# Optimization experiments

Hardware: AMD Instinct MI355X
Metric: run time of the kernel (lower is better)

## Reference

```python
import jax, jax.numpy as jnp
import numpy as np

NUM_BINS = 36
EPS = 1e-12
BASE_DROP, MIN_DROP, MAX_DROP = 0.3, 0.1, 0.6
SENSITIVITY, NORMAL_APE = 4.0, 0.78


def _hann(n):
    # torch.hann_window default (periodic=True): 0.5*(1 - cos(2*pi*k/N))
    return 0.5 - 0.5 * jnp.cos(2.0 * jnp.pi * jnp.arange(n, dtype=jnp.float32) / n)


def compute_ape(images):
    B, C, H, W = images.shape
    mean = jnp.array([0.485, 0.456, 0.406], dtype=images.dtype).reshape(1, 3, 1, 1)
    std = jnp.array([0.229, 0.224, 0.225], dtype=images.dtype).reshape(1, 3, 1, 1)
    wts = jnp.array([0.2989, 0.587, 0.114], dtype=images.dtype).reshape(1, 3, 1, 1)
    gray = ((images * std + mean) * wts).sum(axis=1)  # (B,H,W)
    gray = gray - gray.mean(axis=(1, 2), keepdims=True)
    gray = gray * (_hann(H)[:, None] * _hann(W)[None, :])
    P = jnp.abs(jnp.fft.fft2(gray)) ** 2
    P = jnp.fft.fftshift(P, axes=(1, 2))
    cy, cx = (H - 1) / 2.0, (W - 1) / 2.0
    yy = jnp.arange(H, dtype=jnp.float32)[:, None] - cy
    xx = jnp.arange(W, dtype=jnp.float32)[None, :] - cx
    r = jnp.sqrt(xx ** 2 + yy ** 2)
    theta = (jnp.arctan2(yy, xx) + 2 * jnp.pi) % (2 * jnp.pi)
    r_max = r.max()
    radial_mask = (r >= 0.05 * r_max) & (r <= 0.95 * r_max)
    bin_width = 2 * jnp.pi / NUM_BINS
    idx = jnp.clip((theta / bin_width).astype(jnp.int32), 0, NUM_BINS - 1)  # (H,W)
    # batched masked angular histogram: one segment_sum over B*NUM_BINS segments
    Pm = (P * radial_mask).reshape(B, -1)
    seg = (idx.reshape(-1)[None, :] + NUM_BINS * jnp.arange(B)[:, None]).reshape(-1)
    energy = jax.ops.segment_sum(Pm.reshape(-1), seg, num_segments=B * NUM_BINS)
    energy = energy.reshape(B, NUM_BINS)
    total = energy.sum(axis=1, keepdims=True)
    p = energy / (total + EPS)
    H_theta = -(p * jnp.log(p + EPS)).sum(axis=1)
    ape = jnp.clip(H_theta / np.log(NUM_BINS), 0.0, 1.0)
    return jnp.where(total[:, 0] <= EPS, 0.0, ape)


def ape_to_dropout_prob(ape):
    adj = jnp.tanh((NORMAL_APE - ape) * SENSITIVITY)
    drop = jnp.where(adj >= 0,
                     BASE_DROP + adj * (MAX_DROP - BASE_DROP),
                     BASE_DROP + adj * (BASE_DROP - MIN_DROP))
    return jnp.clip(drop, MIN_DROP, MAX_DROP)


def adaptive_dropout(x, probs, key):
    # per-sample dropout: mask ~ Bernoulli(1-p), scale by 1/(1-p+1e-8)
    p = probs[:, None, None]
    keep = jax.random.bernoulli(key, 1.0 - p, x.shape).astype(x.dtype)
    out = x * keep / (1.0 - p + 1e-8)
    return jnp.where(p > 0, out, x)


def setup_inputs() -> dict:
    key = jax.random.key(0)
    k1, k2, k3, k4 = jax.random.split(key, 4)
    B, N, D, Hf = 64, 256, 768, 768
    images = jax.random.uniform(k1, (B, 3, 448, 448), dtype=jnp.float32)
    x = jax.random.normal(k2, (B, N, D), dtype=jnp.float32)
    w1 = jax.random.normal(k3, (Hf, D), dtype=jnp.float32) * (1.0 / np.sqrt(D))
    w2 = jax.random.normal(k4, (D, Hf), dtype=jnp.float32) * (1.0 / np.sqrt(Hf))
    return {"images": images, "x": x, "w1": w1, "w2": w2}


def reference(images, x, w1, w2):
    ape = compute_ape(images)
    probs = jax.lax.stop_gradient(ape_to_dropout_prob(ape))  # torch casts to python float -> detached
    k0, k1, k2 = jax.random.split(jax.random.key(1), 3)
    h = adaptive_dropout(x, probs, k0)            # input dropout
    h = jnp.einsum('bnd,hd->bnh', h, w1)          # fc1 (bias=False)
    h = jax.nn.gelu(h, approximate=False)         # nn.GELU (exact erf)
    h = adaptive_dropout(h, probs, k1)
    y = jnp.einsum('bnh,dh->bnd', h, w2)          # fc2 (bias=False)
    y = adaptive_dropout(y, probs, k2)
    return y
```

## Files before the change

### kernel.cpp

```cpp
#include <hip/hip_runtime.h>
#include <stdint.h>
#include <math.h>

typedef __attribute__((ext_vector_type(8))) short short8;
typedef __attribute__((ext_vector_type(4))) float floatx4;

#define IMGN 448
#define HW   200704
#define NBATCH 64
#define NBINS 36

#define MFMA(a, b, c) __builtin_amdgcn_mfma_f32_16x16x32_bf16((a), (b), (c), 0, 0, 0)

#define WAITBAR8() asm volatile("s_waitcnt vmcnt(8)\ns_barrier" ::: "memory")
#define WAITBAR6() asm volatile("s_waitcnt vmcnt(6)\ns_barrier" ::: "memory")
#define WAITBAR0() asm volatile("s_waitcnt vmcnt(0)\ns_barrier" ::: "memory")
#define ENDBAR()   asm volatile("s_waitcnt lgkmcnt(0)\ns_barrier" ::: "memory")

#define WS_WIN   0u
#define WS_BINS  4096u
#define WS_TS    24576u
#define WS_BIDX  32768u
#define WS_TW    1048576u
#define TWSZ     401408u
#define WS_W     4194304u
#define WSZ      1179648u
#define WS_REG1  16777216u
#define GSZ      25690112u
#define CBSZ     13762560u
#define XSZ      25165824u
#define WS_REG2  75497472u

__host__ __device__ __forceinline__ uint32_t rotl32(uint32_t v, int r) {
  return (v << r) | (v >> (32 - r));
}
__host__ __device__ __forceinline__ void tf2x32(uint32_t k0, uint32_t k1,
                                                uint32_t x0, uint32_t x1,
                                                uint32_t &o0, uint32_t &o1) {
  uint32_t k2 = k0 ^ k1 ^ 0x1BD11BDAu;
  uint32_t v0 = x0 + k0, v1 = x1 + k1;
#define TFR(r) { v0 += v1; v1 = rotl32(v1, r); v1 ^= v0; }
  TFR(13) TFR(15) TFR(26) TFR(6)   v0 += k1; v1 += k2 + 1u;
  TFR(17) TFR(29) TFR(16) TFR(24)  v0 += k2; v1 += k0 + 2u;
  TFR(13) TFR(15) TFR(26) TFR(6)   v0 += k0; v1 += k1 + 3u;
  TFR(17) TFR(29) TFR(16) TFR(24)  v0 += k1; v1 += k2 + 4u;
  TFR(13) TFR(15) TFR(26) TFR(6)   v0 += k2; v1 += k0 + 5u;
#undef TFR
  o0 = v0; o1 = v1;
}
__device__ __forceinline__ float tf_uniform(uint32_t k0, uint32_t k1, uint32_t idx) {
  uint32_t a, b;
  tf2x32(k0, k1, 0u, idx, a, b);
  uint32_t bits = a ^ b;
  return __uint_as_float((bits >> 9) | 0x3F800000u) - 1.0f;
}

__device__ __forceinline__ unsigned short bf16rne(float v) {
  unsigned u = __float_as_uint(v);
  return (unsigned short)((u + 0x7fffu + ((u >> 16) & 1u)) >> 16);
}
__device__ __forceinline__ void split2(float v, unsigned short &h, unsigned short &l) {
  h = bf16rne(v);
  float fh = __uint_as_float(((unsigned)h) << 16);
  l = bf16rne(v - fh);
}

__device__ __forceinline__ float fast_erf(float x) {
  float ax = fabsf(x);
  float t = 1.0f / (1.0f + 0.3275911f * ax);
  float p = t * (0.254829592f + t * (-0.284496736f + t * (1.421413741f +
            t * (-1.453152027f + t * 1.061405429f))));
  float y = 1.0f - p * __expf(-ax * ax);
  return __uint_as_float((__float_as_uint(y) & 0x7fffffffu) |
                         (__float_as_uint(x) & 0x80000000u));
}

__device__ __forceinline__ void gload16(const void *g, void *l) {
  __builtin_amdgcn_global_load_lds(
      (const __attribute__((address_space(1))) unsigned int *)g,
      (__attribute__((address_space(3))) unsigned int *)l, 16, 0, 0);
}

__global__ __launch_bounds__(256) void k_prep(float *__restrict__ win,
                                              double *__restrict__ bins,
                                              uint8_t *__restrict__ bidx) {
  int t = blockIdx.x * 256 + threadIdx.x;
  int a = t / IMGN, b = t % IMGN;
  double yy = (double)((a + 224) % IMGN) - 223.5;
  double xx = (double)((b + 224) % IMGN) - 223.5;
  double r2 = xx * xx + yy * yy;
  uint8_t idx = 255;
  if (r2 >= 249.76125 && r2 <= 90163.81125) {
    double th = atan2(yy, xx);
    if (th < 0.0) th += 6.283185307179586476925286766559;
    int i = (int)(th / 0.17453292519943295769236907684886);
    if (i > 35) i = 35;
    if (i < 0) i = 0;
    idx = (uint8_t)i;
  }
  bidx[t] = idx;
  if (t < IMGN) {
    double ang = 6.283185307179586476925286766559 * (double)t / 448.0;
    win[t] = (float)(0.5 - 0.5 * cos(ang));
  }
  if (t < NBATCH * NBINS) bins[t] = 0.0;
}

__global__ __launch_bounds__(256) void k_tw(short8 *__restrict__ tch, short8 *__restrict__ tcl,
                                            short8 *__restrict__ tsh, short8 *__restrict__ tsl) {
  int wid = blockIdx.x * 256 + threadIdx.x;
  int lane = wid & 63;
  int tmp = wid >> 6;
  int kb = tmp % 14, mb = tmp / 14;
  int m = mb * 16 + (lane & 15);
  int k0 = kb * 32 + (lane >> 4) * 8;
  short8 ch, cl, sh, sl;
#pragma unroll
  for (int e = 0; e < 8; ++e) {
    int mm = (m * (k0 + e)) % IMGN;
    double ang = -6.283185307179586476925286766559 * (double)mm / 448.0;
    float c = (float)cos(ang), s = (float)sin(ang);
    unsigned short h, l;
    split2(c, h, l); ch[e] = (short)h; cl[e] = (short)l;
    split2(s, h, l); sh[e] = (short)h; sl[e] = (short)l;
  }
  tch[wid] = ch; tcl[wid] = cl; tsh[wid] = sh; tsl[wid] = sl;
}

__global__ __launch_bounds__(256) void k_wconv(const float *__restrict__ w1, const float *__restrict__ w2,
                                               short8 *__restrict__ w1h, short8 *__restrict__ w1l,
                                               short8 *__restrict__ w2h, short8 *__restrict__ w2l) {
  int wid = blockIdx.x * 256 + threadIdx.x;
  const float *src = blockIdx.y ? w2 : w1;
  short8 *dh = blockIdx.y ? w2h : w1h;
  short8 *dl = blockIdx.y ? w2l : w1l;
  int lane = wid & 63;
  int tmp = wid >> 6;
  int kb = tmp % 24, nb = tmp / 24;
  int n = nb * 16 + (lane & 15);
  int k0 = kb * 32 + (lane >> 4) * 8;
  const float *p = src + (size_t)n * 768 + k0;
  short8 vh, vl;
#pragma unroll
  for (int e = 0; e < 8; ++e) {
    unsigned short h, l;
    split2(p[e], h, l);
    vh[e] = (short)h; vl[e] = (short)l;
  }
  dh[wid] = vh; dl[wid] = vl;
}

__global__ __launch_bounds__(256) void k_gprep(const float *__restrict__ img, const float *__restrict__ win,
                                               short8 *__restrict__ gh, short8 *__restrict__ gl) {
  int wid = blockIdx.x * 256 + threadIdx.x;
  int lane = wid & 63;
  int tmp = wid >> 6;
  int kb = tmp % 14, nb = tmp / 14;
  int n = nb * 16 + (lane & 15);
  int b = n / 448, y = n % 448;
  int x0 = kb * 32 + (lane >> 4) * 8;
  const float *p = img + (size_t)b * 3 * HW + y * IMGN + x0;
  float wy = win[y];
  short8 vh, vl;
#pragma unroll
  for (int e = 0; e < 8; ++e) {
    float r = p[e], g = p[HW + e], bl = p[2 * HW + e];
    float t0 = (r * 0.229f + 0.485f) * 0.2989f;
    float t1 = (g * 0.224f + 0.456f) * 0.587f;
    float t2 = (bl * 0.225f + 0.406f) * 0.114f;
    float v = ((t0 + t1) + t2) * wy * win[x0 + e];
    unsigned short h, l;
    split2(v, h, l);
    vh[e] = (short)h; vl[e] = (short)l;
  }
  gh[wid] = vh; gl[wid] = vl;
}

__global__ __launch_bounds__(256) void k_rows(const short8 *__restrict__ tch, const short8 *__restrict__ tcl,
                                              const short8 *__restrict__ tsh, const short8 *__restrict__ tsl,
                                              const short8 *__restrict__ gh, const short8 *__restrict__ gl,
                                              short8 *__restrict__ crh, short8 *__restrict__ crl,
                                              short8 *__restrict__ cih, short8 *__restrict__ cil) {
  __shared__ short8 S[512];
  int orig = blockIdx.x;
  int swz = (orig & 7) * 224 + (orig >> 3);
  int mtg = swz & 3, ntg = swz >> 2;
  int tid = threadIdx.x;
  int lane = tid & 63, w = tid >> 6;
  int g = lane >> 4, c = lane & 15;
  int mt = mtg * 4 + w;
  floatx4 s_c[4] = {}, s_s[4] = {};
  for (int kb = 0; kb < 14; ++kb) {
#pragma unroll
    for (int i = 0; i < 2; ++i) {
      int ch = w * 2 + i;
      const short8 *m0 = (ch >> 2) ? gl : gh;
      int row = ntg * 4 + (ch & 3);
      gload16(m0 + ((size_t)row * 14 + kb) * 64 + lane, (char *)S + ch * 1024);
    }
    int ao = (mt * 14 + kb) * 64 + lane;
    short8 ach = tch[ao], acl = tcl[ao], ash = tsh[ao], asl = tsl[ao];
    __syncthreads();
#pragma unroll
    for (int nt = 0; nt < 4; ++nt) {
      short8 bh = S[nt * 64 + lane];
      short8 bl = S[(4 + nt) * 64 + lane];
      s_c[nt] = MFMA(ach, bh, s_c[nt]);
      s_c[nt] = MFMA(ach, bl, s_c[nt]);
      s_c[nt] = MFMA(acl, bh, s_c[nt]);
      s_s[nt] = MFMA(ash, bh, s_s[nt]);
      s_s[nt] = MFMA(ash, bl, s_s[nt]);
      s_s[nt] = MFMA(asl, bh, s_s[nt]);
    }
    __syncthreads();
  }
#pragma unroll
  for (int nt = 0; nt < 4; ++nt) {
    int nrow = (ntg * 4 + nt) * 16 + c;
    int b = nrow / 448, y = nrow % 448;
    int kb2 = y >> 5;
    int lofs = 16 * ((y & 31) >> 3);
    int e2 = y & 7;
#pragma unroll
    for (int r = 0; r < 4; ++r) {
      int v = mt * 16 + 4 * g + r;
      if (v < 240) {
        int n2 = b * 240 + v;
        size_t word = ((size_t)(n2 >> 4) * 14 + kb2) * 64 + (n2 & 15) + lofs;
        unsigned short h, l;
        split2(s_c[nt][r], h, l);
        ((unsigned short *)crh)[word * 8 + e2] = h;
        ((unsigned short *)crl)[word * 8 + e2] = l;
        split2(s_s[nt][r], h, l);
        ((unsigned short *)cih)[word * 8 + e2] = h;
        ((unsigned short *)cil)[word * 8 + e2] = l;
      }
    }
  }
}

__global__ __launch_bounds__(256) void k_cols(const short8 *__restrict__ tch, const short8 *__restrict__ tcl,
                                              const short8 *__restrict__ tsh, const short8 *__restrict__ tsl,
                                              const short8 *__restrict__ crh, const short8 *__restrict__ crl,
                                              const short8 *__restrict__ cih, const short8 *__restrict__ cil,
                                              const uint8_t *__restrict__ bidx, double *__restrict__ bins) {
  __shared__ short8 S[2][1024];
  __shared__ double lb[72];
  int orig = blockIdx.x;
  int swz = (orig & 7) * 210 + (orig >> 3);
  int mtg = swz % 7, ntg = swz / 7;
  int tid = threadIdx.x;
  if (tid < 72) lb[tid] = 0.0;
  int lane = tid & 63, w = tid >> 6;
  int g = lane >> 4, c = lane & 15;
  int mt = mtg * 4 + w;
  int nt0 = ntg * 4;
  floatx4 s_cc[4] = {}, s_sc[4] = {}, s_ss[4] = {}, s_cs[4] = {};
  short8 aAc, aAcl, aAs, aAsl, aBc, aBcl, aBs, aBsl;

#define C_STAGE(buf, kb) { \
  _Pragma("unroll") for (int i = 0; i < 4; ++i) { \
    int ch = w * 4 + i; int sel = ch >> 2; \
    const short8 *m0 = sel == 0 ? crh : sel == 1 ? crl : sel == 2 ? cih : cil; \
    int row = nt0 + (ch & 3); \
    gload16(m0 + ((size_t)row * 14 + (kb)) * 64 + lane, (char *)&S[buf][0] + ch * 1024); } }
#define C_LOADA(p, kb) { int ao = (mt * 14 + (kb)) * 64 + lane; \
  p##c = tch[ao]; p##cl = tcl[ao]; p##s = tsh[ao]; p##sl = tsl[ao]; }
#define C_COMPUTE(buf, p) { const short8 *Sc = &S[buf][0]; \
  _Pragma("unroll") for (int nt = 0; nt < 4; ++nt) { \
    short8 brh = Sc[nt * 64 + lane]; \
    short8 brl = Sc[(4 + nt) * 64 + lane]; \
    short8 bih = Sc[(8 + nt) * 64 + lane]; \
    short8 bil = Sc[(12 + nt) * 64 + lane]; \
    s_cc[nt] = MFMA(p##c, brh, s_cc[nt]); \
    s_cc[nt] = MFMA(p##c, brl, s_cc[nt]); \
    s_cc[nt] = MFMA(p##cl, brh, s_cc[nt]); \
    s_sc[nt] = MFMA(p##s, brh, s_sc[nt]); \
    s_sc[nt] = MFMA(p##s, brl, s_sc[nt]); \
    s_sc[nt] = MFMA(p##sl, brh, s_sc[nt]); \
    s_ss[nt] = MFMA(p##s, bih, s_ss[nt]); \
    s_ss[nt] = MFMA(p##s, bil, s_ss[nt]); \
    s_ss[nt] = MFMA(p##sl, bih, s_ss[nt]); \
    s_cs[nt] = MFMA(p##c, bih, s_cs[nt]); \
    s_cs[nt] = MFMA(p##c, bil, s_cs[nt]); \
    s_cs[nt] = MFMA(p##cl, bih, s_cs[nt]); } }

  C_STAGE(0, 0); C_LOADA(aA, 0);
  for (int kb = 0; kb < 14; kb += 2) {
    C_STAGE(1, kb + 1); C_LOADA(aB, kb + 1);
    WAITBAR8();
    C_COMPUTE(0, aA);
    ENDBAR();
    if (kb < 12) { C_STAGE(0, kb + 2); C_LOADA(aA, kb + 2); WAITBAR8(); }
    else { WAITBAR0(); }
    C_COMPUTE(1, aB);
    ENDBAR();
  }
  int base_b = (ntg * 64) / 240;
  int cb0 = -1, cb1 = -1, cb2 = -1, cb3 = -1;
  double cv0 = 0.0, cv1 = 0.0, cv2 = 0.0, cv3 = 0.0;
#define PUTBIN(slot_, val_)                                                    \
  { int _s = (slot_); double _v = (val_);                                      \
    if (_s == cb0) cv0 += _v;                                                  \
    else if (_s == cb1) cv1 += _v;                                             \
    else if (_s == cb2) cv2 += _v;                                             \
    else if (_s == cb3) cv3 += _v;                                             \
    else {                                                                     \
      if (cb3 >= 0) atomicAdd(&lb[cb3], cv3);                                  \
      cb3 = cb2; cv3 = cv2; cb2 = cb1; cv2 = cv1;                              \
      cb1 = cb0; cv1 = cv0; cb0 = _s; cv0 = _v;                                \
    } }
#pragma unroll
  for (int nt = 0; nt < 4; ++nt) {
    int n = (nt0 + nt) * 16 + c;
    int v = n % 240;
    int bloc = n / 240 - base_b;
    if (v < 225) {
#pragma unroll
      for (int r = 0; r < 4; ++r) {
        int u = mt * 16 + 4 * g + r;
        float frv = s_cc[nt][r] - s_ss[nt][r];
        float fiv = s_sc[nt][r] + s_cs[nt][r];
        double P = (double)frv * frv + (double)fiv * fiv;
        int i1 = bidx[u * IMGN + v];
        if (i1 < 36) PUTBIN(bloc * 36 + i1, P);
        if (v >= 1 && v <= 223) {
          int i2 = bidx[((IMGN - u) % IMGN) * IMGN + (IMGN - v)];
          if (i2 < 36) PUTBIN(bloc * 36 + i2, P);
        }
      }
    }
  }
  if (cb0 >= 0) atomicAdd(&lb[cb0], cv0);
  if (cb1 >= 0) atomicAdd(&lb[cb1], cv1);
  if (cb2 >= 0) atomicAdd(&lb[cb2], cv2);
  if (cb3 >= 0) atomicAdd(&lb[cb3], cv3);
#undef PUTBIN
  __syncthreads();
  if (tid < 72) {
    int bb = base_b + tid / 36;
    if (bb < NBATCH && lb[tid] != 0.0) atomicAdd(&bins[bb * NBINS + (tid % 36)], lb[tid]);
  }
}

__global__ void k_probs(const double *__restrict__ bins, float *__restrict__ ts) {
  int b = threadIdx.x;
  if (b >= NBATCH) return;
  double T = 0.0;
  for (int i = 0; i < NBINS; ++i) T += bins[b * NBINS + i];
  double H = 0.0;
  for (int i = 0; i < NBINS; ++i) {
    double p = bins[b * NBINS + i] / (T + 1e-12);
    H -= p * log(p + 1e-12);
  }
  double ape = H / 3.5835189384561099;
  if (ape > 1.0) ape = 1.0;
  if (ape < 0.0) ape = 0.0;
  if (T <= 1e-12) ape = 0.0;
  double adj = tanh((0.78 - ape) * 4.0);
  double drop = (adj >= 0.0) ? (0.3 + adj * 0.3) : (0.3 + adj * 0.2);
  if (drop < 0.1) drop = 0.1;
  if (drop > 0.6) drop = 0.6;
  float p32 = (float)drop;
  ts[b] = 1.0f - p32;
  ts[NBATCH + b] = 1.0f / (1.0f - p32 + 1e-8f);
}

__global__ __launch_bounds__(256) void k_dropfrag(const float *__restrict__ x, const float *__restrict__ ts,
                                                  short8 *__restrict__ xh, short8 *__restrict__ xl,
                                                  uint32_t k0, uint32_t k1) {
  int wid = blockIdx.x * 256 + threadIdx.x;
  int lane = wid & 63;
  int tmp = wid >> 6;
  int kb = tmp % 24, mb = tmp / 24;
  int m = mb * 16 + (lane & 15);
  int d0 = kb * 32 + (lane >> 4) * 8;
  int bi = m >> 8;
  float t = ts[bi], s = ts[NBATCH + bi];
  const float *p = x + (size_t)m * 768 + d0;
  short8 vh, vl;
#pragma unroll
  for (int e = 0; e < 8; ++e) {
    uint32_t idx = (uint32_t)m * 768u + (uint32_t)(d0 + e);
    float u = tf_uniform(k0, k1, idx);
    float v = (u < t) ? p[e] * s : 0.0f;
    unsigned short h, l;
    split2(v, h, l);
    vh[e] = (short)h; vl[e] = (short)l;
  }
  xh[wid] = vh; xl[wid] = vl;
}

template <int MODE>
__global__ __launch_bounds__(256) void k_mlp(const short8 *__restrict__ ah, const short8 *__restrict__ al,
                                             const short8 *__restrict__ bh, const short8 *__restrict__ bl,
                                             const float *__restrict__ ts, float *__restrict__ out,
                                             short8 *__restrict__ oh, short8 *__restrict__ ol,
                                             uint32_t k0, uint32_t k1) {
  __shared__ short8 S[2][512];
  int orig = blockIdx.x;
  int swz = (orig & 7) * 192 + (orig >> 3);
  int ntg = swz % 12, mtg = swz / 12;
  int tid = threadIdx.x;
  int lane = tid & 63, w = tid >> 6;
  int g = lane >> 4, c = lane & 15;
  int mt0 = mtg * 8 + w * 2;
  int nt0 = ntg * 4;
  floatx4 acc0[4] = {}, acc1[4] = {};
  short8 aAh0, aAl0, aAh1, aAl1, aBh0, aBl0, aBh1, aBl1;

#define M_STAGE(buf, kb) { \
  _Pragma("unroll") for (int i = 0; i < 2; ++i) { \
    int ch = w * 2 + i; \
    const short8 *m0 = (ch >> 2) ? bl : bh; \
    int row = nt0 + (ch & 3); \
    gload16(m0 + ((size_t)row * 24 + (kb)) * 64 + lane, (char *)&S[buf][0] + ch * 1024); } }
#define M_LOADA(p, kb) { int ao = (mt0 * 24 + (kb)) * 64 + lane; \
  p##h0 = ah[ao]; p##l0 = al[ao]; \
  p##h1 = ah[ao + 24 * 64]; p##l1 = al[ao + 24 * 64]; }
#define M_COMPUTE(buf, p) { const short8 *Sc = &S[buf][0]; \
  _Pragma("unroll") for (int nt = 0; nt < 4; ++nt) { \
    short8 b_h = Sc[nt * 64 + lane]; \
    short8 b_l = Sc[(4 + nt) * 64 + lane]; \
    acc0[nt] = MFMA(p##h0, b_h, acc0[nt]); \
    acc0[nt] = MFMA(p##h0, b_l, acc0[nt]); \
    acc0[nt] = MFMA(p##l0, b_h, acc0[nt]); \
    acc1[nt] = MFMA(p##h1, b_h, acc1[nt]); \
    acc1[nt] = MFMA(p##h1, b_l, acc1[nt]); \
    acc1[nt] = MFMA(p##l1, b_h, acc1[nt]); } }

  M_STAGE(0, 0); M_LOADA(aA, 0);
  for (int kb = 0; kb < 24; kb += 2) {
    M_STAGE(1, kb + 1); M_LOADA(aB, kb + 1);
    WAITBAR6();
    M_COMPUTE(0, aA);
    ENDBAR();
    if (kb < 22) { M_STAGE(0, kb + 2); M_LOADA(aA, kb + 2); WAITBAR6(); }
    else { WAITBAR0(); }
    M_COMPUTE(1, aB);
    ENDBAR();
  }
#define M_EPI(ACC, MT)                                                         \
  {                                                                            \
    _Pragma("unroll") for (int nt = 0; nt < 4; ++nt) {                         \
      int n = (nt0 + nt) * 16 + c;                                             \
      _Pragma("unroll") for (int r = 0; r < 4; ++r) {                          \
        int m = (MT) * 16 + 4 * g + r;                                         \
        float val = ACC[nt][r];                                                \
        if (MODE == 1)                                                         \
          val = 0.5f * val * (1.0f + fast_erf(val * 0.70710678118654752440f)); \
        int bi = m >> 8;                                                       \
        float t = ts[bi], s = ts[NBATCH + bi];                                 \
        uint32_t idx = (uint32_t)m * 768u + (uint32_t)n;                       \
        float u = tf_uniform(k0, k1, idx);                                     \
        val = (u < t) ? val * s : 0.0f;                                        \
        if (MODE == 1) {                                                       \
          unsigned short hh, hl;                                               \
          split2(val, hh, hl);                                                 \
          int kb2 = n >> 5;                                                    \
          int lane2 = (m & 15) + 16 * ((n & 31) >> 3);                         \
          int e2 = n & 7;                                                      \
          size_t word = ((size_t)(m >> 4) * 24 + kb2) * 64 + lane2;            \
          ((unsigned short *)oh)[word * 8 + e2] = hh;                          \
          ((unsigned short *)ol)[word * 8 + e2] = hl;                          \
        } else {                                                               \
          out[(size_t)m * 768 + n] = val;                                      \
        }                                                                      \
      }                                                                        \
    }                                                                          \
  }
  M_EPI(acc0, mt0)
  M_EPI(acc1, mt0 + 1)
#undef M_EPI
}

extern "C" void kernel_launch(void *const *d_in, const int *in_sizes, int n_in,
                              void *d_out, int out_size, void *d_ws, size_t ws_size,
                              hipStream_t stream) {
  (void)in_sizes; (void)n_in; (void)out_size; (void)ws_size;
  const float *images = (const float *)d_in[0];
  const float *x  = (const float *)d_in[1];
  const float *w1 = (const float *)d_in[2];
  const float *w2 = (const float *)d_in[3];

  char *ws = (char *)d_ws;
  float   *win  = (float *)  (ws + WS_WIN);
  double  *bins = (double *) (ws + WS_BINS);
  float   *ts   = (float *)  (ws + WS_TS);
  uint8_t *bidx = (uint8_t *)(ws + WS_BIDX);
  short8  *tch  = (short8 *) (ws + WS_TW + 0 * TWSZ);
  short8  *tcl  = (short8 *) (ws + WS_TW + 1 * TWSZ);
  short8  *tsh  = (short8 *) (ws + WS_TW + 2 * TWSZ);
  short8  *tsl  = (short8 *) (ws + WS_TW + 3 * TWSZ);
  short8  *w1h  = (short8 *) (ws + WS_W + 0 * WSZ);
  short8  *w1l  = (short8 *) (ws + WS_W + 1 * WSZ);
  short8  *w2h  = (short8 *) (ws + WS_W + 2 * WSZ);
  short8  *w2l  = (short8 *) (ws + WS_W + 3 * WSZ);
  short8  *gh   = (short8 *) (ws + WS_REG1 + 0 * GSZ);
  short8  *gl   = (short8 *) (ws + WS_REG1 + 1 * GSZ);
  short8  *xh   = (short8 *) (ws + WS_REG1 + 0 * XSZ);
  short8  *xl   = (short8 *) (ws + WS_REG1 + 1 * XSZ);
  short8  *crh  = (short8 *) (ws + WS_REG2 + 0 * CBSZ);
  short8  *crl  = (short8 *) (ws + WS_REG2 + 1 * CBSZ);
  short8  *cih  = (short8 *) (ws + WS_REG2 + 2 * CBSZ);
  short8  *cil  = (short8 *) (ws + WS_REG2 + 3 * CBSZ);
  short8  *hh_  = (short8 *) (ws + WS_REG2 + 0 * XSZ);
  short8  *hl_  = (short8 *) (ws + WS_REG2 + 1 * XSZ);
  float   *yout = (float *)d_out;

  uint32_t keys[6];
  tf2x32(0u, 1u, 0u, 0u, keys[0], keys[1]);
  tf2x32(0u, 1u, 0u, 1u, keys[2], keys[3]);
  tf2x32(0u, 1u, 0u, 2u, keys[4], keys[5]);

  k_prep<<<784, 256, 0, stream>>>(win, bins, bidx);
  k_tw<<<98, 256, 0, stream>>>(tch, tcl, tsh, tsl);
  k_wconv<<<dim3(288, 2), 256, 0, stream>>>(w1, w2, w1h, w1l, w2h, w2l);
  k_gprep<<<6272, 256, 0, stream>>>(images, win, gh, gl);
  k_rows<<<1792, 256, 0, stream>>>(tch, tcl, tsh, tsl, gh, gl, crh, crl, cih, cil);
  k_cols<<<1680, 256, 0, stream>>>(tch, tcl, tsh, tsl, crh, crl, cih, cil, bidx, bins);
  k_probs<<<1, 64, 0, stream>>>(bins, ts);
  k_dropfrag<<<6144, 256, 0, stream>>>(x, ts, xh, xl, keys[0], keys[1]);
  k_mlp<1><<<1536, 256, 0, stream>>>(xh, xl, w1h, w1l, ts, yout, hh_, hl_, keys[2], keys[3]);
  k_mlp<2><<<1536, 256, 0, stream>>>(hh_, hl_, w2h, w2l, ts, yout, hh_, hl_, keys[4], keys[5]);
}
```

Measured before the change: 394.6 us.

## Use two-wave k_cols blocks with two M-tiles per wave, single-buffered LDS

k_cols now runs 128-thread blocks where each wave computes two 16-row M-tiles instead of one. This doubles register accumulators and reuses each LDS-staged B fragment across twice as many MFMAs. The double-buffered LDS pipeline with hand-tuned vmcnt waits is replaced by a single buffer and plain __syncthreads, so global loads no longer overlap compute within a block. The change trades load/compute overlap and occupancy (more VGPRs per wave) for fewer LDS reads per MFMA and lower LDS usage.

```diff
diff --git a/kernel.cpp b/kernel.cpp
--- a/kernel.cpp
+++ b/kernel.cpp
@@ -12,7 +12,6 @@
 
 #define MFMA(a, b, c) __builtin_amdgcn_mfma_f32_16x16x32_bf16((a), (b), (c), 0, 0, 0)
 
-#define WAITBAR8() asm volatile("s_waitcnt vmcnt(8)\ns_barrier" ::: "memory")
 #define WAITBAR6() asm volatile("s_waitcnt vmcnt(6)\ns_barrier" ::: "memory")
 #define WAITBAR0() asm volatile("s_waitcnt vmcnt(0)\ns_barrier" ::: "memory")
 #define ENDBAR()   asm volatile("s_waitcnt lgkmcnt(0)\ns_barrier" ::: "memory")
@@ -239,12 +238,12 @@
   }
 }
 
-__global__ __launch_bounds__(256) void k_cols(const short8 *__restrict__ tch, const short8 *__restrict__ tcl,
+__global__ __launch_bounds__(128) void k_cols(const short8 *__restrict__ tch, const short8 *__restrict__ tcl,
                                               const short8 *__restrict__ tsh, const short8 *__restrict__ tsl,
                                               const short8 *__restrict__ crh, const short8 *__restrict__ crl,
                                               const short8 *__restrict__ cih, const short8 *__restrict__ cil,
                                               const uint8_t *__restrict__ bidx, double *__restrict__ bins) {
-  __shared__ short8 S[2][1024];
+  __shared__ short8 S[1024];
   __shared__ double lb[72];
   int orig = blockIdx.x;
   int swz = (orig & 7) * 210 + (orig >> 3);
@@ -253,48 +252,55 @@
   if (tid < 72) lb[tid] = 0.0;
   int lane = tid & 63, w = tid >> 6;
   int g = lane >> 4, c = lane & 15;
-  int mt = mtg * 4 + w;
+  int mt0 = mtg * 4 + w * 2;
   int nt0 = ntg * 4;
-  floatx4 s_cc[4] = {}, s_sc[4] = {}, s_ss[4] = {}, s_cs[4] = {};
-  short8 aAc, aAcl, aAs, aAsl, aBc, aBcl, aBs, aBsl;
-
-#define C_STAGE(buf, kb) { \
-  _Pragma("unroll") for (int i = 0; i < 4; ++i) { \
-    int ch = w * 4 + i; int sel = ch >> 2; \
-    const short8 *m0 = sel == 0 ? crh : sel == 1 ? crl : sel == 2 ? cih : cil; \
-    int row = nt0 + (ch & 3); \
-    gload16(m0 + ((size_t)row * 14 + (kb)) * 64 + lane, (char *)&S[buf][0] + ch * 1024); } }
-#define C_LOADA(p, kb) { int ao = (mt * 14 + (kb)) * 64 + lane; \
-  p##c = tch[ao]; p##cl = tcl[ao]; p##s = tsh[ao]; p##sl = tsl[ao]; }
-#define C_COMPUTE(buf, p) { const short8 *Sc = &S[buf][0]; \
-  _Pragma("unroll") for (int nt = 0; nt < 4; ++nt) { \
-    short8 brh = Sc[nt * 64 + lane]; \
-    short8 brl = Sc[(4 + nt) * 64 + lane]; \
-    short8 bih = Sc[(8 + nt) * 64 + lane]; \
-    short8 bil = Sc[(12 + nt) * 64 + lane]; \
-    s_cc[nt] = MFMA(p##c, brh, s_cc[nt]); \
-    s_cc[nt] = MFMA(p##c, brl, s_cc[nt]); \
-    s_cc[nt] = MFMA(p##cl, brh, s_cc[nt]); \
-    s_sc[nt] = MFMA(p##s, brh, s_sc[nt]); \
-    s_sc[nt] = MFMA(p##s, brl, s_sc[nt]); \
-    s_sc[nt] = MFMA(p##sl, brh, s_sc[nt]); \
-    s_ss[nt] = MFMA(p##s, bih, s_ss[nt]); \
-    s_ss[nt] = MFMA(p##s, bil, s_ss[nt]); \
-    s_ss[nt] = MFMA(p##sl, bih, s_ss[nt]); \
-    s_cs[nt] = MFMA(p##c, bih, s_cs[nt]); \
-    s_cs[nt] = MFMA(p##c, bil, s_cs[nt]); \
-    s_cs[nt] = MFMA(p##cl, bih, s_cs[nt]); } }
-
-  C_STAGE(0, 0); C_LOADA(aA, 0);
-  for (int kb = 0; kb < 14; kb += 2) {
-    C_STAGE(1, kb + 1); C_LOADA(aB, kb + 1);
-    WAITBAR8();
-    C_COMPUTE(0, aA);
-    ENDBAR();
-    if (kb < 12) { C_STAGE(0, kb + 2); C_LOADA(aA, kb + 2); WAITBAR8(); }
-    else { WAITBAR0(); }
-    C_COMPUTE(1, aB);
-    ENDBAR();
+  floatx4 cc0[4] = {}, sc0[4] = {}, ss0[4] = {}, cs0[4] = {};
+  floatx4 cc1[4] = {}, sc1[4] = {}, ss1[4] = {}, cs1[4] = {};
+  for (int kb = 0; kb < 14; ++kb) {
+#pragma unroll
+    for (int i = 0; i < 8; ++i) {
+      int ch = w * 8 + i;
+      int sel = ch >> 2;
+      const short8 *m0 = sel == 0 ? crh : sel == 1 ? crl : sel == 2 ? cih : cil;
+      int row = nt0 + (ch & 3);
+      gload16(m0 + ((size_t)row * 14 + kb) * 64 + lane, (char *)S + ch * 1024);
+    }
+    int ao = (mt0 * 14 + kb) * 64 + lane;
+    short8 c0 = tch[ao], l0 = tcl[ao], s0 = tsh[ao], z0 = tsl[ao];
+    short8 c1 = tch[ao + 896], l1 = tcl[ao + 896], s1 = tsh[ao + 896], z1 = tsl[ao + 896];
+    __syncthreads();
+#pragma unroll
+    for (int nt = 0; nt < 4; ++nt) {
+      short8 brh = S[nt * 64 + lane];
+      short8 brl = S[(4 + nt) * 64 + lane];
+      short8 bih = S[(8 + nt) * 64 + lane];
+      short8 bil = S[(12 + nt) * 64 + lane];
+      cc0[nt] = MFMA(c0, brh, cc0[nt]);
+      cc0[nt] = MFMA(c0, brl, cc0[nt]);
+      cc0[nt] = MFMA(l0, brh, cc0[nt]);
+      sc0[nt] = MFMA(s0, brh, sc0[nt]);
+      sc0[nt] = MFMA(s0, brl, sc0[nt]);
+      sc0[nt] = MFMA(z0, brh, sc0[nt]);
+      ss0[nt] = MFMA(s0, bih, ss0[nt]);
+      ss0[nt] = MFMA(s0, bil, ss0[nt]);
+      ss0[nt] = MFMA(z0, bih, ss0[nt]);
+      cs0[nt] = MFMA(c0, bih, cs0[nt]);
+      cs0[nt] = MFMA(c0, bil, cs0[nt]);
+      cs0[nt] = MFMA(l0, bih, cs0[nt]);
+      cc1[nt] = MFMA(c1, brh, cc1[nt]);
+      cc1[nt] = MFMA(c1, brl, cc1[nt]);
+      cc1[nt] = MFMA(l1, brh, cc1[nt]);
+      sc1[nt] = MFMA(s1, brh, sc1[nt]);
+      sc1[nt] = MFMA(s1, brl, sc1[nt]);
+      sc1[nt] = MFMA(z1, brh, sc1[nt]);
+      ss1[nt] = MFMA(s1, bih, ss1[nt]);
+      ss1[nt] = MFMA(s1, bil, ss1[nt]);
+      ss1[nt] = MFMA(z1, bih, ss1[nt]);
+      cs1[nt] = MFMA(c1, bih, cs1[nt]);
+      cs1[nt] = MFMA(c1, bil, cs1[nt]);
+      cs1[nt] = MFMA(l1, bih, cs1[nt]);
+    }
+    __syncthreads();
   }
   int base_b = (ntg * 64) / 240;
   int cb0 = -1, cb1 = -1, cb2 = -1, cb3 = -1;
@@ -310,27 +316,31 @@
       cb3 = cb2; cv3 = cv2; cb2 = cb1; cv2 = cv1;                              \
       cb1 = cb0; cv1 = cv0; cb0 = _s; cv0 = _v;                                \
     } }
-#pragma unroll
-  for (int nt = 0; nt < 4; ++nt) {
-    int n = (nt0 + nt) * 16 + c;
-    int v = n % 240;
-    int bloc = n / 240 - base_b;
-    if (v < 225) {
-#pragma unroll
-      for (int r = 0; r < 4; ++r) {
-        int u = mt * 16 + 4 * g + r;
-        float frv = s_cc[nt][r] - s_ss[nt][r];
-        float fiv = s_sc[nt][r] + s_cs[nt][r];
-        double P = (double)frv * frv + (double)fiv * fiv;
-        int i1 = bidx[u * IMGN + v];
-        if (i1 < 36) PUTBIN(bloc * 36 + i1, P);
-        if (v >= 1 && v <= 223) {
-          int i2 = bidx[((IMGN - u) % IMGN) * IMGN + (IMGN - v)];
-          if (i2 < 36) PUTBIN(bloc * 36 + i2, P);
-        }
-      }
-    }
-  }
+#define C_EPI(CC, SC, SS, CS, MT)                                              \
+  {                                                                            \
+    _Pragma("unroll") for (int nt = 0; nt < 4; ++nt) {                         \
+      int n = (nt0 + nt) * 16 + c;                                             \
+      int v = n % 240;                                                         \
+      int bloc = n / 240 - base_b;                                             \
+      if (v < 225) {                                                           \
+        _Pragma("unroll") for (int r = 0; r < 4; ++r) {                        \
+          int u = (MT) * 16 + 4 * g + r;                                       \
+          float frv = CC[nt][r] - SS[nt][r];                                   \
+          float fiv = SC[nt][r] + CS[nt][r];                                   \
+          double P = (double)frv * frv + (double)fiv * fiv;                    \
+          int i1 = bidx[u * IMGN + v];                                         \
+          if (i1 < 36) PUTBIN(bloc * 36 + i1, P);                              \
+          if (v >= 1 && v <= 223) {                                            \
+            int i2 = bidx[((IMGN - u) % IMGN) * IMGN + (IMGN - v)];            \
+            if (i2 < 36) PUTBIN(bloc * 36 + i2, P);                            \
+          }                                                                    \
+        }                                                                      \
+      }                                                                        \
+    }                                                                          \
+  }
+  C_EPI(cc0, sc0, ss0, cs0, mt0)
+  C_EPI(cc1, sc1, ss1, cs1, mt0 + 1)
+#undef C_EPI
   if (cb0 >= 0) atomicAdd(&lb[cb0], cv0);
   if (cb1 >= 0) atomicAdd(&lb[cb1], cv1);
   if (cb2 >= 0) atomicAdd(&lb[cb2], cv2);
@@ -518,7 +528,7 @@
   k_wconv<<<dim3(288, 2), 256, 0, stream>>>(w1, w2, w1h, w1l, w2h, w2l);
   k_gprep<<<6272, 256, 0, stream>>>(images, win, gh, gl);
   k_rows<<<1792, 256, 0, stream>>>(tch, tcl, tsh, tsl, gh, gl, crh, crl, cih, cil);
-  k_cols<<<1680, 256, 0, stream>>>(tch, tcl, tsh, tsl, crh, crl, cih, cil, bidx, bins);
+  k_cols<<<1680, 128, 0, stream>>>(tch, tcl, tsh, tsl, crh, crl, cih, cil, bidx, bins);
   k_probs<<<1, 64, 0, stream>>>(bins, ts);
   k_dropfrag<<<6144, 256, 0, stream>>>(x, ts, xh, xl, keys[0], keys[1]);
   k_mlp<1><<<1536, 256, 0, stream>>>(xh, xl, w1h, w1l, ts, yout, hh_, hl_, keys[2], keys[3]);
```

Result: slower. 470.2 us (+19.2%).
